# Kernel optimization log

Hardware: AMD Instinct MI355X
Metric: run time of the kernel (lower is better)

## Reference

```python
import jax, jax.numpy as jnp
import numpy as np

E, H, B, S = 1024, 16, 8, 512
D = E // H
GRU_BIAS = 2.0  # config['gru_bias']
LN_EPS = 1e-5


def _pos_encoding(seq_len, dim):
    # Transformer-XL style relative positions seq_len-1 .. 0
    pos = jnp.arange(seq_len - 1, -1, -1, dtype=jnp.float32)
    inv_freq = 1.0 / (10000.0 ** (jnp.arange(0, dim, 2, dtype=jnp.float32) / dim))
    ang = pos[:, None] * inv_freq[None, :]              # [S, E/2]
    return jnp.concatenate([jnp.sin(ang), jnp.cos(ang)], axis=-1)  # [S, E]


def _layer_norm(x, g, b):
    m = x.mean(-1, keepdims=True)
    v = ((x - m) ** 2).mean(-1, keepdims=True)
    return (x - m) * jax.lax.rsqrt(v + LN_EPS) * g + b


def _rel_shift(x):
    # x: [B, H, S, S] -> Transformer-XL relative shift
    b, h, s, _ = x.shape
    x = jnp.pad(x, ((0, 0), (0, 0), (0, 0), (1, 0)))
    x = x.reshape(b, h, s + 1, s)[:, :, 1:, :]
    return x


def _gru_gate(x, y, Wr, Ur, Wz, Uz, Wg, Ug):
    # GTrXL gating: r, z gates + candidate h; z biased toward identity by GRU_BIAS
    r = jax.nn.sigmoid(y @ Wr.T + x @ Ur.T)
    z = jax.nn.sigmoid(y @ Wz.T + x @ Uz.T - GRU_BIAS)
    h = jnp.tanh(y @ Wg.T + (r * x) @ Ug.T)
    return (1.0 - z) * x + z * h


def setup_inputs() -> dict:
    rng = jax.random.key(0)
    ks = iter(jax.random.split(rng, 64))
    W = lambda *shape: jax.random.normal(next(ks), shape, jnp.float32) * 0.02
    inp = {
        "query": jax.random.normal(next(ks), (B, S, E), jnp.float32),
        "key": jax.random.normal(next(ks), (B, S, E), jnp.float32),
        "value": jax.random.normal(next(ks), (B, S, E), jnp.float32),
        "mask": jnp.tril(jnp.ones((S, S), dtype=bool)),
        "ln1_g": jnp.ones((E,), jnp.float32), "ln1_b": jnp.zeros((E,), jnp.float32),
        "ln2_g": jnp.ones((E,), jnp.float32), "ln2_b": jnp.zeros((E,), jnp.float32),
        "Wq": W(E, E), "bq": jnp.zeros((E,), jnp.float32),
        "Wk": W(E, E), "bk": jnp.zeros((E,), jnp.float32),
        "Wv": W(E, E), "bv": jnp.zeros((E,), jnp.float32),
        "Wp": W(E, E),
        "Wo": W(E, E), "bo": jnp.zeros((E,), jnp.float32),
        "u_bias": W(H, D), "v_bias": W(H, D),
        "g1_Wr": W(E, E), "g1_Ur": W(E, E), "g1_Wz": W(E, E),
        "g1_Uz": W(E, E), "g1_Wg": W(E, E), "g1_Ug": W(E, E),
        "g2_Wr": W(E, E), "g2_Ur": W(E, E), "g2_Wz": W(E, E),
        "g2_Uz": W(E, E), "g2_Wg": W(E, E), "g2_Ug": W(E, E),
        "fc_W": W(E, E), "fc_b": jnp.zeros((E,), jnp.float32),
    }
    return inp


def reference(query, key, value, mask,
              ln1_g, ln1_b, ln2_g, ln2_b,
              Wq, bq, Wk, bk, Wv, bv, Wp, Wo, bo, u_bias, v_bias,
              g1_Wr, g1_Ur, g1_Wz, g1_Uz, g1_Wg, g1_Ug,
              g2_Wr, g2_Ur, g2_Wz, g2_Uz, g2_Wg, g2_Ug,
              fc_W, fc_b):
    b, s, e = query.shape
    norm_q = _layer_norm(query, ln1_g, ln1_b)
    norm_k = _layer_norm(key, ln1_g, ln1_b)

    q = (norm_q @ Wq.T + bq).reshape(b, s, H, D)
    k = (norm_k @ Wk.T + bk).reshape(b, s, H, D)
    v = (norm_k @ Wv.T + bv).reshape(b, s, H, D)
    r = (_pos_encoding(s, e) @ Wp.T).reshape(s, H, D)      # relative pos keys

    # content term (q + u) k^T and position term (q + v) R^T with rel-shift
    AC = jnp.einsum('bshd,bthd->bhst', q + u_bias, k)
    BD = _rel_shift(jnp.einsum('bshd,thd->bhst', q + v_bias, r))
    score = (AC + BD) / jnp.sqrt(jnp.float32(D))
    score = jnp.where(mask[None, None, :, :], score, jnp.float32(-1e9))
    attn = jax.nn.softmax(score, axis=-1)
    Y = jnp.einsum('bhst,bthd->bshd', attn, v).reshape(b, s, e) @ Wo.T + bo

    out = _gru_gate(query, Y, g1_Wr, g1_Ur, g1_Wz, g1_Uz, g1_Wg, g1_Ug)
    Ef = jax.nn.relu(_layer_norm(out, ln2_g, ln2_b) @ fc_W.T + fc_b)
    out = _gru_gate(out, Ef, g2_Wr, g2_Ur, g2_Wz, g2_Uz, g2_Wg, g2_Ug)
    return out
```

## Files before the change

### kernel.cpp

```cpp
#include <hip/hip_runtime.h>

typedef unsigned short u16;
typedef __attribute__((ext_vector_type(8))) short short8;
typedef __attribute__((ext_vector_type(4))) float f32x4;

#define DEVFN __device__ __forceinline__

constexpr int Bc = 8, Sc = 512, Ec = 1024, Hc = 16, Dc = 64;

DEVFN u16 f2b(float f) {
  union { float f; unsigned u; } a; a.f = f;
  unsigned u = a.u;
  u += 0x7fffu + ((u >> 16) & 1u);
  return (u16)(u >> 16);
}
DEVFN unsigned pack2(float a, float b) {
  return (unsigned)f2b(a) | ((unsigned)f2b(b) << 16);
}
DEVFN float wred_sum(float v) {
  #pragma unroll
  for (int o = 32; o; o >>= 1) v += __shfl_xor(v, o, 64);
  return v;
}
DEVFN void gload16(const void* g, void* l) {
  __builtin_amdgcn_global_load_lds(
      (const __attribute__((address_space(1))) void*)g,
      (__attribute__((address_space(3))) void*)l, 16, 0, 0);
}

struct PtrBundle { const float* src[18]; u16* dst[18]; };

__global__ __launch_bounds__(256) void cvtw_kernel(PtrBundle pb)
{
  int w = blockIdx.y;
  int i = blockIdx.x * 256 + threadIdx.x;
  float4 v = ((const float4*)pb.src[w])[i];
  uint2 o; o.x = pack2(v.x, v.y); o.y = pack2(v.z, v.w);
  ((uint2*)pb.dst[w])[i] = o;
}

struct GemmSeg {
  const u16* A1; const u16* A2;
  const u16* W1; const u16* W2;
  const float* bias;
  const float* bu; const float* bv;
  const float* xF;
  const float* zF;
  u16* o16a; u16* o16b;
  float* oF;
  int epi;
};
struct GemmDesc { GemmSeg seg[3]; };

template<int TN>
__global__ __launch_bounds__(256) void gemm_f(GemmDesc dd)
{
  constexpr int NI = TN / 32;
  constexpr int BPS = 1024 / TN;
  __shared__ u16 lA[2][128 * 32];
  __shared__ u16 lB[2][TN * 32];
  const int tid = threadIdx.x;
  const GemmSeg s = dd.seg[blockIdx.y / BPS];
  const int n0 = (blockIdx.y % BPS) * TN;
  const int m0 = blockIdx.x * 128;
  const int wid = tid >> 6, lane = tid & 63;
  const int wm = (wid >> 1) * 64, wn = (wid & 1) * (TN / 2);
  const int c15 = lane & 15, g8 = (lane >> 4) * 8;
  const int arow = tid >> 2, ac8 = (tid & 3) * 8;

  f32x4 acc[4][NI];
  #pragma unroll
  for (int mi = 0; mi < 4; ++mi)
    #pragma unroll
    for (int ni = 0; ni < NI; ++ni) acc[mi][ni] = {0.f, 0.f, 0.f, 0.f};

  const int nst = (s.A2 ? 2 : 1) * 32;

  auto stage = [&](int buf, int st) {
    int sg = st >> 5, k0 = (st & 31) << 5;
    const u16* Abase = (sg ? s.A2 : s.A1) + (size_t)m0 * 1024;
    const u16* Wbase = (sg ? s.W2 : s.W1) + (size_t)n0 * 1024;
    gload16(Abase + (size_t)arow * 1024 + k0 + ac8,        &lA[buf][tid * 8]);
    gload16(Abase + (size_t)(arow + 64) * 1024 + k0 + ac8, &lA[buf][2048 + tid * 8]);
    gload16(Wbase + (size_t)arow * 1024 + k0 + ac8,        &lB[buf][tid * 8]);
    if constexpr (TN == 128)
      gload16(Wbase + (size_t)(arow + 64) * 1024 + k0 + ac8, &lB[buf][2048 + tid * 8]);
  };

  stage(0, 0);
  stage(1, 1);

  for (int st = 0; st < nst; ++st) {
    const int cur = st & 1;
    if (st + 1 < nst) {
      if constexpr (TN == 128) asm volatile("s_waitcnt vmcnt(4)" ::: "memory");
      else                     asm volatile("s_waitcnt vmcnt(3)" ::: "memory");
    } else {
      asm volatile("s_waitcnt vmcnt(0)" ::: "memory");
    }
    __builtin_amdgcn_s_barrier();

    short8 afr[4], bfr[NI];
    #pragma unroll
    for (int mi = 0; mi < 4; ++mi)
      afr[mi] = *(const short8*)&lA[cur][(wm + mi * 16 + c15) * 32 + g8];
    #pragma unroll
    for (int ni = 0; ni < NI; ++ni)
      bfr[ni] = *(const short8*)&lB[cur][(wn + ni * 16 + c15) * 32 + g8];
    asm volatile("s_waitcnt lgkmcnt(0)" ::: "memory");
    __builtin_amdgcn_sched_barrier(0);
    __builtin_amdgcn_s_barrier();
    __builtin_amdgcn_sched_barrier(0);
    if (st + 2 < nst) stage(cur, st + 2);

    #pragma unroll
    for (int mi = 0; mi < 4; ++mi)
      #pragma unroll
      for (int ni = 0; ni < NI; ++ni)
        acc[mi][ni] = __builtin_amdgcn_mfma_f32_16x16x32_bf16(
            afr[mi], bfr[ni], acc[mi][ni], 0, 0, 0);
  }

  const int colb = n0 + wn + c15;
  const int rowb = m0 + wm + (lane >> 4) * 4;
  #pragma unroll
  for (int ni = 0; ni < NI; ++ni) {
    int col = colb + ni * 16;
    float bb = s.bias ? s.bias[col] : 0.f;
    float bu = 0.f, bvv = 0.f;
    if (s.epi == 1) { bu = s.bu[col]; bvv = s.bv[col]; }
    int hI = col >> 6, dI = col & 63;
    int kcd = (dI >> 5) & 1, gd = (dI >> 3) & 3, ed = dI & 7;
    int ntd = dI >> 4, c15d = dI & 15;
    #pragma unroll
    for (int mi = 0; mi < 4; ++mi) {
      int row0 = rowb + mi * 16;
      size_t off0 = (size_t)row0 * 1024 + col;
      float v4[4];
      #pragma unroll
      for (int q = 0; q < 4; ++q) v4[q] = acc[mi][ni][q] + bb;
      switch (s.epi) {
        case 0:
          #pragma unroll
          for (int q = 0; q < 4; ++q) s.o16a[off0 + (size_t)q * 1024] = f2b(v4[q]);
          break;
        case 1:
          #pragma unroll
          for (int q = 0; q < 4; ++q) {
            int ri = row0 + q;
            size_t off = ((size_t)hI << 18) +
                         (((size_t)(((ri >> 4) * 2 + kcd) * 16 + (ri & 15)) * 4 + gd) << 3) + ed;
            s.o16a[off] = f2b((v4[q] + bu)  * 0.125f);
            s.o16b[off] = f2b((v4[q] + bvv) * 0.125f);
          }
          break;
        case 2:
          #pragma unroll
          for (int q = 0; q < 4; ++q) s.oF[off0 + (size_t)q * 1024] = v4[q];
          break;
        case 3:
          #pragma unroll
          for (int q = 0; q < 4; ++q) {
            size_t off = off0 + (size_t)q * 1024;
            float sg1 = 1.f / (1.f + __expf(-v4[q]));
            s.o16a[off] = f2b(sg1 * s.xF[off]);
          }
          break;
        case 4:
          #pragma unroll
          for (int q = 0; q < 4; ++q) {
            size_t off = off0 + (size_t)q * 1024;
            float z = 1.f / (1.f + __expf(-(s.zF[off] - 2.f)));
            float r = (1.f - z) * s.xF[off] + z * tanhf(v4[q]);
            s.oF[off] = r;
            if (s.o16a) s.o16a[off] = f2b(r);
          }
          break;
        case 5:
          #pragma unroll
          for (int q = 0; q < 4; ++q) s.o16a[off0 + (size_t)q * 1024] = f2b(fmaxf(v4[q], 0.f));
          break;
        case 6: {
          int bI = row0 >> 9, j = row0 & 511;
          int kt = j >> 6, jj = j & 63;
          int kcj = jj >> 5, gj = (jj >> 3) & 3, e0 = jj & 7;
          size_t off = ((size_t)((bI * 16 + hI) * 8 + kt) << 12) +
                       (((size_t)((ntd * 2 + kcj) * 16 + c15d) * 4 + gj) << 3) + e0;
          uint2 o; o.x = pack2(v4[0], v4[1]); o.y = pack2(v4[2], v4[3]);
          *(uint2*)(s.o16a + off) = o;
        } break;
        case 7:
          #pragma unroll
          for (int q = 0; q < 4; ++q) {
            int rj = row0 + q;
            int bI = rj >> 9, kt = (rj >> 6) & 7, jr = rj & 63;
            size_t off = ((size_t)((bI * 16 + hI) * 8 + kt) << 12) +
                         (((size_t)(((jr >> 4) * 2 + kcd) * 16 + (jr & 15)) * 4 + gd) << 3) + ed;
            s.o16a[off] = f2b(v4[q]);
          }
          break;
        case 8:
          #pragma unroll
          for (int q = 0; q < 4; ++q) {
            int t = row0 + q;
            size_t off = ((size_t)hI << 14) +
                         (((size_t)(((t >> 4) * 2 + kcd) * 16 + (t & 15)) * 4 + gd) << 3) + ed;
            s.o16a[off] = f2b(v4[q]);
          }
          break;
      }
    }
  }
}

__global__ __launch_bounds__(256) void ln_kernel(
    const float* __restrict__ x, const float* __restrict__ g,
    const float* __restrict__ bb, u16* __restrict__ out,
    u16* __restrict__ out2)
{
  const int row = blockIdx.x, t = threadIdx.x;
  float4 xv = ((const float4*)x)[(size_t)row * 256 + t];
  float s  = xv.x + xv.y + xv.z + xv.w;
  float s2 = xv.x * xv.x + xv.y * xv.y + xv.z * xv.z + xv.w * xv.w;
  s = wred_sum(s); s2 = wred_sum(s2);
  __shared__ float sh[8];
  int wid = t >> 6, lane = t & 63;
  if (lane == 0) { sh[wid] = s; sh[4 + wid] = s2; }
  __syncthreads();
  s  = sh[0] + sh[1] + sh[2] + sh[3];
  s2 = sh[4] + sh[5] + sh[6] + sh[7];
  float mean = s * (1.f / 1024.f);
  float var  = s2 * (1.f / 1024.f) - mean * mean;
  float rstd = rsqrtf(var + 1e-5f);
  float4 gv = ((const float4*)g)[t];
  float4 bv = ((const float4*)bb)[t];
  uint2 o;
  o.x = pack2((xv.x - mean) * rstd * gv.x + bv.x,
              (xv.y - mean) * rstd * gv.y + bv.y);
  o.y = pack2((xv.z - mean) * rstd * gv.z + bv.z,
              (xv.w - mean) * rstd * gv.w + bv.w);
  *(uint2*)&out[(size_t)row * 1024 + t * 4] = o;
  if (out2) {
    uint2 o2; o2.x = pack2(xv.x, xv.y); o2.y = pack2(xv.z, xv.w);
    *(uint2*)&out2[(size_t)row * 1024 + t * 4] = o2;
  }
}

__global__ __launch_bounds__(256) void posenc_kernel(u16* __restrict__ out)
{
  int idx = blockIdx.x * 256 + threadIdx.x;
  int i = idx >> 9, f = idx & 511;
  float pos = (float)(Sc - 1 - i);
  float invf = expf((float)f * -0.017988946039016f);
  float ang = pos * invf;
  out[(size_t)i * 1024 + f]       = f2b(sinf(ang));
  out[(size_t)i * 1024 + 512 + f] = f2b(cosf(ang));
}

__global__ __launch_bounds__(256) void attn_mfma(
    const u16* __restrict__ quF, const u16* __restrict__ qvF,
    const u16* __restrict__ PK, const u16* __restrict__ PVT,
    const u16* __restrict__ RF, u16* __restrict__ out)
{
  __shared__ u16 lK[2][4096];
  __shared__ u16 lVT[2][4096];
  __shared__ u16 PW[4][16 * 72];

  const int tid = threadIdx.x;
  const int wave = tid >> 6, lane = tid & 63;
  const int g = lane >> 4, c15 = lane & 15;
  const int x = blockIdx.x;
  const int h = blockIdx.y, b = blockIdx.z;
  const int qA = x, qB = 7 - x;

  const size_t pkbase = (size_t)(b * 16 + h) << 15;
  const size_t qhead  = (size_t)h << 18;
  const size_t rhead  = (size_t)h << 14;
  const size_t bh_off = ((size_t)b * Sc) * Ec + h * Dc;
  const int fchunk = (c15 * 4 + g) * 8;

  u16* pw = PW[wave];

  auto stage = [&](int buf, int kt) {
    const u16* ks = PK  + pkbase + ((size_t)kt << 12);
    const u16* vs = PVT + pkbase + ((size_t)kt << 12);
    gload16(ks + tid * 8,        &lK[buf][tid * 8]);
    gload16(ks + 2048 + tid * 8, &lK[buf][2048 + tid * 8]);
    gload16(vs + tid * 8,        &lVT[buf][tid * 8]);
    gload16(vs + 2048 + tid * 8, &lVT[buf][2048 + tid * 8]);
  };

  short8 qa[2], va[2];
  int i0w = qA * 64 + wave * 16;
  {
    int i16g = b * 32 + (i0w >> 4);
    #pragma unroll
    for (int kc = 0; kc < 2; ++kc) {
      size_t off = qhead + ((size_t)(i16g * 2 + kc) * 64) * 8 + fchunk;
      qa[kc] = *(const short8*)(quF + off);
      va[kc] = *(const short8*)(qvF + off);
    }
  }

  f32x4 oacc[4];
  #pragma unroll
  for (int t = 0; t < 4; ++t) oacc[t] = {0.f, 0.f, 0.f, 0.f};
  float m[4], l[4];
  #pragma unroll
  for (int q = 0; q < 4; ++q) { m[q] = -1e30f; l[q] = 0.f; }

  stage(0, 0);
  asm volatile("s_waitcnt vmcnt(0)" ::: "memory");
  __syncthreads();

  for (int s2 = 0; s2 < 9; ++s2) {
    const int buf = s2 & 1;
    const int kt = (s2 <= x) ? s2 : (s2 - x - 1);
    const int j0 = kt * 64;
    if (s2 < 8) {
      int ns = s2 + 1;
      stage(buf ^ 1, (ns <= x) ? ns : (ns - x - 1));
    }

    f32x4 ac[4];
    #pragma unroll
    for (int t = 0; t < 4; ++t) ac[t] = {0.f, 0.f, 0.f, 0.f};
    __builtin_amdgcn_s_setprio(1);
    #pragma unroll
    for (int kc = 0; kc < 2; ++kc)
      #pragma unroll
      for (int nt = 0; nt < 4; ++nt) {
        short8 kb = *(const short8*)&lK[buf][(nt * 2 + kc) * 512 + fchunk];
        ac[nt] = __builtin_amdgcn_mfma_f32_16x16x32_bf16(qa[kc], kb, ac[nt], 0, 0, 0);
      }

    const int t016 = (496 - i0w + j0) >> 4;
    f32x4 e5[5];
    #pragma unroll
    for (int t = 0; t < 5; ++t) e5[t] = {0.f, 0.f, 0.f, 0.f};
    #pragma unroll
    for (int kc = 0; kc < 2; ++kc)
      #pragma unroll
      for (int nt = 0; nt < 5; ++nt) {
        int t16 = t016 + nt; t16 = t16 > 31 ? 31 : t16;
        short8 rb = *(const short8*)(RF + rhead + (size_t)(t16 * 2 + kc) * 512 + fchunk);
        e5[nt] = __builtin_amdgcn_mfma_f32_16x16x32_bf16(va[kc], rb, e5[nt], 0, 0, 0);
      }
    __builtin_amdgcn_s_setprio(0);

    float rot[5][4];
    #pragma unroll
    for (int q = 0; q < 4; ++q) {
      int src = (lane & 48) | ((15 - (g * 4 + q) + c15) & 15);
      #pragma unroll
      for (int nt = 0; nt < 5; ++nt)
        rot[nt][q] = __shfl(e5[nt][q], src, 64);
    }

    float s[4][4];
    #pragma unroll
    for (int ct = 0; ct < 4; ++ct) {
      int jcol = j0 + ct * 16 + c15;
      #pragma unroll
      for (int q = 0; q < 4; ++q) {
        int r = g * 4 + q;
        int u = 15 - r + c15;
        float bd = (u >> 4) ? rot[ct + 1][q] : rot[ct][q];
        float sv = ac[ct][q] + bd;
        s[ct][q] = (jcol <= i0w + r) ? sv : -1e30f;
      }
    }

    float mnew[4], csc[4];
    #pragma unroll
    for (int q = 0; q < 4; ++q) {
      float mx = fmaxf(fmaxf(s[0][q], s[1][q]), fmaxf(s[2][q], s[3][q]));
      #pragma unroll
      for (int o = 8; o; o >>= 1) mx = fmaxf(mx, __shfl_xor(mx, o, 64));
      mnew[q] = fmaxf(m[q], mx);
      csc[q] = __expf(m[q] - mnew[q]);
      m[q] = mnew[q];
    }
    float rs[4] = {0.f, 0.f, 0.f, 0.f};
    float p[4][4];
    #pragma unroll
    for (int ct = 0; ct < 4; ++ct)
      #pragma unroll
      for (int q = 0; q < 4; ++q) {
        p[ct][q] = __expf(s[ct][q] - mnew[q]);
        rs[q] += p[ct][q];
      }
    #pragma unroll
    for (int q = 0; q < 4; ++q) {
      float t = rs[q];
      #pragma unroll
      for (int o = 8; o; o >>= 1) t += __shfl_xor(t, o, 64);
      l[q] = l[q] * csc[q] + t;
      #pragma unroll
      for (int ct = 0; ct < 4; ++ct) oacc[ct][q] *= csc[q];
    }

    #pragma unroll
    for (int ct = 0; ct < 4; ++ct)
      #pragma unroll
      for (int q = 0; q < 4; ++q)
        pw[(g * 4 + q) * 72 + ct * 16 + c15] = f2b(p[ct][q]);

    __builtin_amdgcn_s_setprio(1);
    #pragma unroll
    for (int kc = 0; kc < 2; ++kc) {
      short8 pa = *(const short8*)&pw[c15 * 72 + kc * 32 + g * 8];
      #pragma unroll
      for (int nt = 0; nt < 4; ++nt) {
        short8 vb8 = *(const short8*)&lVT[buf][(nt * 2 + kc) * 512 + fchunk];
        oacc[nt] = __builtin_amdgcn_mfma_f32_16x16x32_bf16(pa, vb8, oacc[nt], 0, 0, 0);
      }
    }
    __builtin_amdgcn_s_setprio(0);

    if (s2 == x) {
      #pragma unroll
      for (int q = 0; q < 4; ++q) {
        float rl = 1.f / l[q];
        size_t ro = bh_off + (size_t)(i0w + g * 4 + q) * Ec;
        #pragma unroll
        for (int ct = 0; ct < 4; ++ct)
          out[ro + ct * 16 + c15] = f2b(oacc[ct][q] * rl);
      }
      i0w = qB * 64 + wave * 16;
      int i16g = b * 32 + (i0w >> 4);
      #pragma unroll
      for (int kc = 0; kc < 2; ++kc) {
        size_t off = qhead + ((size_t)(i16g * 2 + kc) * 64) * 8 + fchunk;
        qa[kc] = *(const short8*)(quF + off);
        va[kc] = *(const short8*)(qvF + off);
      }
      #pragma unroll
      for (int t = 0; t < 4; ++t) oacc[t] = {0.f, 0.f, 0.f, 0.f};
      #pragma unroll
      for (int q = 0; q < 4; ++q) { m[q] = -1e30f; l[q] = 0.f; }
    }

    asm volatile("s_waitcnt vmcnt(0)" ::: "memory");
    __syncthreads();
  }

  #pragma unroll
  for (int q = 0; q < 4; ++q) {
    float rl = 1.f / l[q];
    size_t ro = bh_off + (size_t)(i0w + g * 4 + q) * Ec;
    #pragma unroll
    for (int ct = 0; ct < 4; ++ct)
      out[ro + ct * 16 + c15] = f2b(oacc[ct][q] * rl);
  }
}

extern "C" void kernel_launch(void* const* d_in, const int* in_sizes, int n_in,
                              void* d_out, int out_size, void* d_ws, size_t ws_size,
                              hipStream_t stream) {
  (void)in_sizes; (void)n_in; (void)out_size; (void)ws_size;

  const float* query = (const float*)d_in[0];
  const float* key   = (const float*)d_in[1];
  const float* ln1_g = (const float*)d_in[4];
  const float* ln1_b = (const float*)d_in[5];
  const float* ln2_g = (const float*)d_in[6];
  const float* ln2_b = (const float*)d_in[7];
  const float* Wq = (const float*)d_in[8];   const float* bq = (const float*)d_in[9];
  const float* Wk = (const float*)d_in[10];  const float* bk = (const float*)d_in[11];
  const float* Wv = (const float*)d_in[12];  const float* bv_in = (const float*)d_in[13];
  const float* Wp = (const float*)d_in[14];
  const float* Wo = (const float*)d_in[15];  const float* bo = (const float*)d_in[16];
  const float* u_bias = (const float*)d_in[17];
  const float* v_bias = (const float*)d_in[18];
  const float* fc_W = (const float*)d_in[31]; const float* fc_b = (const float*)d_in[32];

  const size_t MB = 1ull << 20;
  char* ws = (char*)d_ws;
  u16* wb[18];
  for (int i = 0; i < 18; ++i) wb[i] = (u16*)(ws + (size_t)i * 2 * MB);
  u16*   normq16 = (u16*)(ws + 36 * MB);
  u16*   normk16 = (u16*)(ws + 44 * MB);
  u16*   xq16    = (u16*)(ws + 52 * MB);
  u16*   pos16   = (u16*)(ws + 60 * MB);
  u16*   rF16    = (u16*)(ws + 61 * MB);
  u16*   quF16   = (u16*)(ws + 62 * MB);
  u16*   qvF16   = (u16*)(ws + 70 * MB);
  u16*   pk16    = (u16*)(ws + 78 * MB);
  u16*   pvt16   = (u16*)(ws + 86 * MB);
  float* out1    = (float*)(ws + 94 * MB);
  u16*   att16   = normq16;
  u16*   Y16     = normk16;
  u16*   rx16    = normq16;
  u16*   out116  = quF16;
  u16*   Ef16    = qvF16;
  u16*   ln2o16  = xq16;
  float* tB      = (float*)pk16;

  PtrBundle pb;
  const float* wsrc[18] = {Wq, Wk, Wv, Wp, Wo, fc_W,
                           (const float*)d_in[19], (const float*)d_in[20],
                           (const float*)d_in[21], (const float*)d_in[22],
                           (const float*)d_in[23], (const float*)d_in[24],
                           (const float*)d_in[25], (const float*)d_in[26],
                           (const float*)d_in[27], (const float*)d_in[28],
                           (const float*)d_in[29], (const float*)d_in[30]};
  for (int i = 0; i < 18; ++i) { pb.src[i] = wsrc[i]; pb.dst[i] = wb[i]; }
  cvtw_kernel<<<dim3(1024, 18), 256, 0, stream>>>(pb);

  ln_kernel<<<4096, 256, 0, stream>>>(query, ln1_g, ln1_b, normq16, xq16);
  ln_kernel<<<4096, 256, 0, stream>>>(key,   ln1_g, ln1_b, normk16, nullptr);
  posenc_kernel<<<1024, 256, 0, stream>>>(pos16);

  GemmSeg z{}; GemmDesc d;

  d.seg[0] = z; d.seg[0].A1 = normq16; d.seg[0].W1 = wb[0]; d.seg[0].bias = bq;
  d.seg[0].bu = u_bias; d.seg[0].bv = v_bias;
  d.seg[0].o16a = quF16; d.seg[0].o16b = qvF16; d.seg[0].epi = 1;
  d.seg[1] = z; d.seg[1].A1 = normk16; d.seg[1].W1 = wb[1]; d.seg[1].bias = bk;
  d.seg[1].o16a = pk16; d.seg[1].epi = 7;
  d.seg[2] = z; d.seg[2].A1 = normk16; d.seg[2].W1 = wb[2]; d.seg[2].bias = bv_in;
  d.seg[2].o16a = pvt16; d.seg[2].epi = 6;
  gemm_f<128><<<dim3(32, 24), 256, 0, stream>>>(d);

  d.seg[0] = z; d.seg[0].A1 = pos16; d.seg[0].W1 = wb[3];
  d.seg[0].o16a = rF16; d.seg[0].epi = 8;
  gemm_f<64><<<dim3(4, 16), 256, 0, stream>>>(d);

  attn_mfma<<<dim3(4, 16, 8), 256, 0, stream>>>(quF16, qvF16, pk16, pvt16,
                                                rF16, att16);

  d.seg[0] = z; d.seg[0].A1 = att16; d.seg[0].W1 = wb[4]; d.seg[0].bias = bo;
  d.seg[0].o16a = Y16; d.seg[0].epi = 0;
  gemm_f<64><<<dim3(32, 16), 256, 0, stream>>>(d);

  d.seg[0] = z; d.seg[0].A1 = Y16; d.seg[0].A2 = xq16;
  d.seg[0].W1 = wb[6]; d.seg[0].W2 = wb[7];
  d.seg[0].xF = query; d.seg[0].o16a = rx16; d.seg[0].epi = 3;
  d.seg[1] = z; d.seg[1].A1 = Y16; d.seg[1].A2 = xq16;
  d.seg[1].W1 = wb[8]; d.seg[1].W2 = wb[9];
  d.seg[1].oF = tB; d.seg[1].epi = 2;
  gemm_f<128><<<dim3(32, 16), 256, 0, stream>>>(d);

  d.seg[0] = z; d.seg[0].A1 = Y16; d.seg[0].A2 = rx16;
  d.seg[0].W1 = wb[10]; d.seg[0].W2 = wb[11];
  d.seg[0].xF = query; d.seg[0].zF = tB;
  d.seg[0].oF = out1; d.seg[0].o16a = out116; d.seg[0].epi = 4;
  gemm_f<64><<<dim3(32, 16), 256, 0, stream>>>(d);

  ln_kernel<<<4096, 256, 0, stream>>>(out1, ln2_g, ln2_b, ln2o16, nullptr);
  d.seg[0] = z; d.seg[0].A1 = ln2o16; d.seg[0].W1 = wb[5]; d.seg[0].bias = fc_b;
  d.seg[0].o16a = Ef16; d.seg[0].epi = 5;
  gemm_f<64><<<dim3(32, 16), 256, 0, stream>>>(d);

  d.seg[0] = z; d.seg[0].A1 = Ef16; d.seg[0].A2 = out116;
  d.seg[0].W1 = wb[12]; d.seg[0].W2 = wb[13];
  d.seg[0].xF = out1; d.seg[0].o16a = rx16; d.seg[0].epi = 3;
  d.seg[1] = z; d.seg[1].A1 = Ef16; d.seg[1].A2 = out116;
  d.seg[1].W1 = wb[14]; d.seg[1].W2 = wb[15];
  d.seg[1].oF = tB; d.seg[1].epi = 2;
  gemm_f<128><<<dim3(32, 16), 256, 0, stream>>>(d);

  d.seg[0] = z; d.seg[0].A1 = Ef16; d.seg[0].A2 = rx16;
  d.seg[0].W1 = wb[16]; d.seg[0].W2 = wb[17];
  d.seg[0].xF = out1; d.seg[0].zF = tB;
  d.seg[0].oF = (float*)d_out; d.seg[0].epi = 4;
  gemm_f<64><<<dim3(32, 16), 256, 0, stream>>>(d);
}
```

Baseline: 390.4 us.

## XOR-swizzle LDS tiles in GEMM and attention; remap GEMM workgroup order

Applies an XOR swizzle to the 16-byte chunk index when staging A/B tiles in the GEMM and K/V^T tiles in the attention kernel, with matching swizzled read offsets. This is meant to remove LDS bank conflicts on the short8 fragment reads. The GEMM also remaps its linear workgroup id into a strided order to change which tiles run together, aiming for better L2 reuse. The swizzle changes global-load source addresses, so correctness depends on the source and read swizzles matching exactly. The workgroup remap assumes the workgroup count is divisible by 8.

```diff
diff --git a/kernel.cpp b/kernel.cpp
--- a/kernel.cpp
+++ b/kernel.cpp
@@ -60,13 +60,22 @@
   __shared__ u16 lA[2][128 * 32];
   __shared__ u16 lB[2][TN * 32];
   const int tid = threadIdx.x;
-  const GemmSeg s = dd.seg[blockIdx.y / BPS];
-  const int n0 = (blockIdx.y % BPS) * TN;
-  const int m0 = blockIdx.x * 128;
+
+  const int nwg = gridDim.x * gridDim.y;
+  const int lid = blockIdx.y * gridDim.x + blockIdx.x;
+  const int swzid = (lid & 7) * (nwg >> 3) + (lid >> 3);
+  const int bx = swzid % gridDim.x;
+  const int by = swzid / gridDim.x;
+
+  const GemmSeg s = dd.seg[by / BPS];
+  const int n0 = (by % BPS) * TN;
+  const int m0 = bx * 128;
   const int wid = tid >> 6, lane = tid & 63;
   const int wm = (wid >> 1) * 64, wn = (wid & 1) * (TN / 2);
-  const int c15 = lane & 15, g8 = (lane >> 4) * 8;
-  const int arow = tid >> 2, ac8 = (tid & 3) * 8;
+  const int c15 = lane & 15, g = lane >> 4;
+  const int arow = tid >> 2;
+  const int ac8 = (((tid & 3) ^ ((tid >> 3) & 3))) * 8;
+  const int gs8 = (g ^ ((c15 >> 1) & 3)) * 8;
 
   f32x4 acc[4][NI];
   #pragma unroll
@@ -103,10 +112,10 @@
     short8 afr[4], bfr[NI];
     #pragma unroll
     for (int mi = 0; mi < 4; ++mi)
-      afr[mi] = *(const short8*)&lA[cur][(wm + mi * 16 + c15) * 32 + g8];
+      afr[mi] = *(const short8*)&lA[cur][(wm + mi * 16 + c15) * 32 + gs8];
     #pragma unroll
     for (int ni = 0; ni < NI; ++ni)
-      bfr[ni] = *(const short8*)&lB[cur][(wn + ni * 16 + c15) * 32 + g8];
+      bfr[ni] = *(const short8*)&lB[cur][(wn + ni * 16 + c15) * 32 + gs8];
     asm volatile("s_waitcnt lgkmcnt(0)" ::: "memory");
     __builtin_amdgcn_sched_barrier(0);
     __builtin_amdgcn_s_barrier();
@@ -277,17 +286,19 @@
   const size_t qhead  = (size_t)h << 18;
   const size_t rhead  = (size_t)h << 14;
   const size_t bh_off = ((size_t)b * Sc) * Ec + h * Dc;
-  const int fchunk = (c15 * 4 + g) * 8;
+  const int fchunk  = (c15 * 4 + g) * 8;
+  const int fchunkS = (c15 * 4 + (g ^ ((c15 >> 1) & 3))) * 8;
+  const int src8 = (tid ^ ((tid >> 3) & 3)) * 8;
 
   u16* pw = PW[wave];
 
   auto stage = [&](int buf, int kt) {
     const u16* ks = PK  + pkbase + ((size_t)kt << 12);
     const u16* vs = PVT + pkbase + ((size_t)kt << 12);
-    gload16(ks + tid * 8,        &lK[buf][tid * 8]);
-    gload16(ks + 2048 + tid * 8, &lK[buf][2048 + tid * 8]);
-    gload16(vs + tid * 8,        &lVT[buf][tid * 8]);
-    gload16(vs + 2048 + tid * 8, &lVT[buf][2048 + tid * 8]);
+    gload16(ks + src8,        &lK[buf][tid * 8]);
+    gload16(ks + 2048 + src8, &lK[buf][2048 + tid * 8]);
+    gload16(vs + src8,        &lVT[buf][tid * 8]);
+    gload16(vs + 2048 + src8, &lVT[buf][2048 + tid * 8]);
   };
 
   short8 qa[2], va[2];
@@ -330,7 +341,7 @@
     for (int kc = 0; kc < 2; ++kc)
       #pragma unroll
       for (int nt = 0; nt < 4; ++nt) {
-        short8 kb = *(const short8*)&lK[buf][(nt * 2 + kc) * 512 + fchunk];
+        short8 kb = *(const short8*)&lK[buf][(nt * 2 + kc) * 512 + fchunkS];
         ac[nt] = __builtin_amdgcn_mfma_f32_16x16x32_bf16(qa[kc], kb, ac[nt], 0, 0, 0);
       }
 
@@ -412,7 +423,7 @@
       short8 pa = *(const short8*)&pw[c15 * 72 + kc * 32 + g * 8];
       #pragma unroll
       for (int nt = 0; nt < 4; ++nt) {
-        short8 vb8 = *(const short8*)&lVT[buf][(nt * 2 + kc) * 512 + fchunk];
+        short8 vb8 = *(const short8*)&lVT[buf][(nt * 2 + kc) * 512 + fchunkS];
         oacc[nt] = __builtin_amdgcn_mfma_f32_16x16x32_bf16(pa, vb8, oacc[nt], 0, 0, 0);
       }
     }
```

Measured after the change: 416.6 us. 1.07x slower.
